# Optimization experiments

Hardware: AMD Instinct MI355X
Metric: run time of the kernel (lower is better)

## Reference

```python
import jax, jax.numpy as jnp
import numpy as np

B, S, HID = 2, 1024, 2048
H, D, KV = 32, 64, 8          # query heads, head dim, kv heads (GQA)
INNER = H * D                 # 2048
KV_DIM = KV * D               # 512


def setup_inputs() -> dict:
    key = jax.random.key(0)
    ks = jax.random.split(key, 12)
    s = 0.02
    return {
        "query": jax.random.normal(ks[0], (B, S, HID), jnp.float32),
        "key": jax.random.normal(ks[1], (B, S, HID), jnp.float32),
        "value": jax.random.normal(ks[2], (B, S, HID), jnp.float32),
        "mask": jnp.zeros((B, 1, S, S), jnp.float32),
        "position_bias": jax.random.normal(ks[3], (1, H, S, S), jnp.float32),
        "Wq": jax.random.normal(ks[4], (HID, INNER), jnp.float32) * s,
        "bq": jnp.zeros((INNER,), jnp.float32),
        "Wk": jax.random.normal(ks[5], (HID, KV_DIM), jnp.float32) * s,
        "bk": jnp.zeros((KV_DIM,), jnp.float32),
        "Wv": jax.random.normal(ks[6], (HID, KV_DIM), jnp.float32) * s,
        "bv": jnp.zeros((KV_DIM,), jnp.float32),
        "Wo": jax.random.normal(ks[7], (INNER, HID), jnp.float32) * s,
        "bo": jnp.zeros((HID,), jnp.float32),
    }


def reference(query, key, value, mask, position_bias, Wq, bq, Wk, bk, Wv, bv, Wo, bo):
    # projections (torch nn.Linear equivalent, weights stored [in,out])
    q = (query @ Wq + bq).reshape(B, S, H, D)     # [B,S,H,D]
    k = (key @ Wk + bk).reshape(B, S, KV, D)      # [B,S,KV,D]
    v = (value @ Wv + bv).reshape(B, S, KV, D)
    rep = H // KV
    k = jnp.repeat(k, rep, axis=2)                # GQA repeat_kv -> [B,S,H,D]
    v = jnp.repeat(v, rep, axis=2)
    scores = jnp.einsum("bqhd,bkhd->bhqk", q, k)  # [B,H,S,S]
    scores = (scores + position_bias) * (1.0 / jnp.sqrt(jnp.float32(D)))
    scores = scores + mask
    probs = jax.nn.softmax(scores.astype(jnp.float32), axis=-1).astype(q.dtype)
    out = jnp.einsum("bhqk,bkhd->bqhd", probs, v).reshape(B, S, INNER)
    return out @ Wo + bo                          # [B,S,HID]
```

## Files before the change

kernel.cpp:

```cpp
#include <hip/hip_runtime.h>
#include <stdint.h>


#define DEVI __device__ __forceinline__

typedef __attribute__((ext_vector_type(8))) short bf16x8;
typedef __attribute__((ext_vector_type(4))) float f32x4;
typedef __attribute__((ext_vector_type(4))) float flt4;
typedef __attribute__((ext_vector_type(8))) unsigned short u16x8;
typedef __attribute__((ext_vector_type(4))) unsigned short u16x4;

DEVI unsigned short f2bf(float f){
  union{float f;uint32_t u;}v; v.f=f;
  uint32_t u=v.u;
  u += 0x7FFFu + ((u>>16)&1u);
  return (unsigned short)(u>>16);
}

DEVI uint32_t cvt_pk_bf16(float lo, float hi){
  uint32_t r;
  asm("v_cvt_pk_bf16_f32 %0, %1, %2" : "=v"(r) : "v"(lo), "v"(hi));
  return r;
}

DEVI float fexp2(float x){
#if __has_builtin(__builtin_amdgcn_exp2f)
  return __builtin_amdgcn_exp2f(x);
#else
  return exp2f(x);
#endif
}

DEVI void gload16(const void* g, void* l){
  __builtin_amdgcn_global_load_lds((const __attribute__((address_space(1))) void*)g,
                                   (__attribute__((address_space(3))) void*)l, 16, 0, 0);
}

__global__ void prep_k(const float* __restrict__ q, const float* __restrict__ k,
                       const float* __restrict__ v,
                       unsigned short* __restrict__ qb, unsigned short* __restrict__ kb,
                       unsigned short* __restrict__ vb,
                       const float* __restrict__ Wq, const float* __restrict__ Wk,
                       const float* __restrict__ Wv, const float* __restrict__ Wo,
                       unsigned short* __restrict__ WqT, unsigned short* __restrict__ WkT,
                       unsigned short* __restrict__ WvT, unsigned short* __restrict__ WoT){
  __shared__ float tile[64][65];
  int bid = blockIdx.x;
  if (bid < 6144){
    int z = bid>>11;
    int i = (bid&2047)*256 + threadIdx.x;
    const float* src = z==0 ? q : (z==1 ? k : v);
    unsigned short* dst = z==0 ? qb : (z==1 ? kb : vb);
    const flt4* s = (const flt4*)src;
    flt4 a = s[2*i], b = s[2*i+1];
    u16x8 o;
    o[0]=f2bf(a.x); o[1]=f2bf(a.y); o[2]=f2bf(a.z); o[3]=f2bf(a.w);
    o[4]=f2bf(b.x); o[5]=f2bf(b.y); o[6]=f2bf(b.z); o[7]=f2bf(b.w);
    ((u16x8*)dst)[i] = o;
    return;
  }
  int id = bid - 6144;
  const int K = 2048;
  const float* W; unsigned short* WT; int N, tt;
  if (id < 1024)      { W=Wq; WT=WqT; N=2048; tt=id; }
  else if (id < 1280) { W=Wk; WT=WkT; N=512;  tt=id-1024; }
  else if (id < 1536) { W=Wv; WT=WvT; N=512;  tt=id-1280; }
  else                { W=Wo; WT=WoT; N=2048; tt=id-1536; }
  int sh = (N==2048) ? 5 : 3;
  int n0 = (tt & ((1<<sh)-1))*64, k0 = (tt >> sh)*64;
  int t = threadIdx.x;
  int r = t>>4, c4 = (t&15)*4;
  #pragma unroll
  for (int i=0;i<4;i++){
    flt4 vv = *(const flt4*)&W[(size_t)(k0 + r + i*16)*N + n0 + c4];
    tile[r+i*16][c4+0]=vv.x; tile[r+i*16][c4+1]=vv.y; tile[r+i*16][c4+2]=vv.z; tile[r+i*16][c4+3]=vv.w;
  }
  __syncthreads();
  #pragma unroll
  for (int i=0;i<4;i++){
    int rn = r + i*16;
    u16x4 o;
    o[0]=f2bf(tile[c4+0][rn]); o[1]=f2bf(tile[c4+1][rn]);
    o[2]=f2bf(tile[c4+2][rn]); o[3]=f2bf(tile[c4+3][rn]);
    *(u16x4*)&WT[(size_t)(n0+rn)*K + k0 + c4] = o;
  }
}

#define GEMM12864_KSTEP(A_, BT_, K_)                                           \
    __syncthreads();                                                           \
    _Pragma("unroll")                                                          \
    for (int j=0;j<4;j++){                                                     \
      int cid = (j*4+w)*64 + l;                                                \
      int row = cid>>3, sl = cid&7;                                            \
      int gsl = sl ^ (row&7);                                                  \
      gload16(&A_[(size_t)(m0+row)*K_ + k0 + gsl*8], &As[(j*4+w)*512]);        \
    }                                                                          \
    _Pragma("unroll")                                                          \
    for (int j=0;j<2;j++){                                                     \
      int cid = (j*4+w)*64 + l;                                                \
      int row = cid>>3, sl = cid&7;                                            \
      int gsl = sl ^ (row&7);                                                  \
      gload16(&BT_[(size_t)(n0+row)*K_ + k0 + gsl*8], &Bs[(j*4+w)*512]);       \
    }                                                                          \
    __syncthreads();                                                           \
    _Pragma("unroll")                                                          \
    for (int kk=0;kk<2;kk++){                                                  \
      bf16x8 af[2], bfv[4];                                                    \
      _Pragma("unroll")                                                        \
      for (int mt=0;mt<2;mt++){                                                \
        int row = wr+mt*16+lq;                                                 \
        af[mt] = *(const bf16x8*)&As[row*64 + (((kk*4+lg)^(lq&7))*8)];         \
      }                                                                        \
      _Pragma("unroll")                                                        \
      for (int nt=0;nt<4;nt++){                                                \
        int row = nt*16+lq;                                                    \
        bfv[nt] = *(const bf16x8*)&Bs[row*64 + (((kk*4+lg)^(lq&7))*8)];        \
      }                                                                        \
      _Pragma("unroll")                                                        \
      for (int mt=0;mt<2;mt++)                                                 \
        _Pragma("unroll")                                                      \
        for (int nt=0;nt<4;nt++)                                               \
          acc[mt][nt] = __builtin_amdgcn_mfma_f32_16x16x32_bf16(af[mt], bfv[nt], acc[mt][nt], 0,0,0); \
    }

__global__ __launch_bounds__(256,3) void qkv128(const unsigned short* __restrict__ qbf,
    const unsigned short* __restrict__ kbf, const unsigned short* __restrict__ vbf,
    const unsigned short* __restrict__ WqT, const unsigned short* __restrict__ WkT,
    const unsigned short* __restrict__ WvT,
    const float* __restrict__ bq, const float* __restrict__ bk, const float* __restrict__ bv,
    unsigned short* __restrict__ Qp, unsigned short* __restrict__ Kp, unsigned short* __restrict__ VTb){
  __shared__ unsigned short As[128*64];
  __shared__ unsigned short Bs[64*64];
  const int K = 2048;
  int id = blockIdx.x;
  const unsigned short *A, *BT; const float* bias; int N, op, tt;
  if (id < 512)      { op=0; A=qbf; BT=WqT; bias=bq; N=2048; tt=id; }
  else if (id < 640) { op=1; A=kbf; BT=WkT; bias=bk; N=512;  tt=id-512; }
  else               { op=2; A=vbf; BT=WvT; bias=bv; N=512;  tt=id-640; }
  int sh = (N==2048) ? 5 : 3;
  int n0 = (tt & ((1<<sh)-1))*64, m0 = (tt >> sh)*128;
  int t = threadIdx.x, w = t>>6, l = t&63;
  int lq = l&15, lg = l>>4;
  int wr = w*32;
  f32x4 acc[2][4] = {};
  for (int k0=0;k0<K;k0+=64){
    GEMM12864_KSTEP(A, BT, K)
  }
  #pragma unroll
  for (int nt=0;nt<4;nt++){
    int col = n0 + nt*16 + lq;
    float bvl = bias[col];
    #pragma unroll
    for (int mt=0;mt<2;mt++){
      #pragma unroll
      for (int r=0;r<4;r++){
        int row = m0 + wr + mt*16 + lg*4 + r;
        float v = acc[mt][nt][r] + bvl;
        if (op==0)      Qp[(size_t)row*2048 + col] = f2bf(v);
        else if (op==1) Kp[(size_t)row*512 + col] = f2bf(v);
        else {
          int b = row>>10, s = row&1023;
          VTb[((size_t)(b*512 + col)<<10) + s] = f2bf(v);
        }
      }
    }
  }
}

__global__ __launch_bounds__(256,3) void oproj128(const unsigned short* __restrict__ A,
    const unsigned short* __restrict__ BT, const float* __restrict__ bias,
    float* __restrict__ Cout){
  __shared__ unsigned short As[128*64];
  __shared__ unsigned short Bs[64*64];
  const int K = 2048, N = 2048;
  int n0 = blockIdx.x*64, m0 = blockIdx.y*128;
  int t = threadIdx.x, w = t>>6, l = t&63;
  int lq = l&15, lg = l>>4;
  int wr = w*32;
  f32x4 acc[2][4] = {};
  for (int k0=0;k0<K;k0+=64){
    GEMM12864_KSTEP(A, BT, K)
  }
  #pragma unroll
  for (int nt=0;nt<4;nt++){
    int col = n0 + nt*16 + lq;
    float bvl = bias[col];
    #pragma unroll
    for (int mt=0;mt<2;mt++){
      #pragma unroll
      for (int r=0;r<4;r++){
        int row = m0 + wr + mt*16 + lg*4 + r;
        Cout[(size_t)row*N + col] = acc[mt][nt][r] + bvl;
      }
    }
  }
}

__global__ __launch_bounds__(512,4) void attn_k(const unsigned short* __restrict__ Q,
    const unsigned short* __restrict__ Kp, const unsigned short* __restrict__ VT,
    const float* __restrict__ pbias, const float* __restrict__ mask,
    unsigned short* __restrict__ Oout){
  __shared__ unsigned short Ks[2][4096];
  __shared__ unsigned short VTs[2][4096];
  __shared__ float Ms[2][2048];
  __shared__ unsigned short Pb[8][1024];
  int t=threadIdx.x, w=t>>6, l=t&63;
  int phys = blockIdx.x;
  int lin = (phys&7)*64 + (phys>>3);
  int qb = lin>>4, kv = (lin>>1)&7, b = lin&1;
  int h = kv*4 + (w&3);
  int qhalf = w>>2;
  int lq = l&15, lg = l>>4;
  int q0 = qb*32 + qhalf*16;
  int mr = qhalf*16 + lq;
  bf16x8 qf0, qf1;
  {
    const unsigned short* qp = &Q[((size_t)(b*1024 + q0 + lq))*2048 + h*64 + lg*8];
    qf0 = *(const bf16x8*)qp;
    qf1 = *(const bf16x8*)(qp + 32);
  }
  const float* pbase  = &pbias[((size_t)h*1024 + (q0+lq))*1024];
  const float* maskWG = &mask [((size_t)(b*1024 + qb*32))*1024];
  f32x4 oacc[4] = {};
  float psum = 0.f;
  const float L2E   = 1.4426950408889634f;
  const float SCL2E = 0.125f*1.4426950408889634f;
  const float NFM   = -16.0f*1.4426950408889634f;
  unsigned short* pw = &Pb[w][0];
  int swz = (lq&7)<<3;

  flt4 RA[4], RB[4], comb[4];

#define ATTN_STAGE(buf_, kt_)                                                           \
  {                                                                                     \
    int c = w*64 + l;                                                                   \
    int krow = c>>3, ksl = (c&7)^(krow&7);                                              \
    gload16(&Kp[((size_t)(b*1024 + (kt_)*64 + krow))*512 + kv*64 + ksl*8], &Ks[buf_][w*512]);          \
    gload16(&VT[((size_t)(b*512 + kv*64 + krow))*1024 + (size_t)((kt_)*64 + ksl*8)], &VTs[buf_][w*512]);\
    int mrow = c>>4, msl = (c&15)^(mrow&7);                                             \
    gload16(&maskWG[(size_t)mrow*1024 + (kt_)*64 + msl*4], &Ms[buf_][w*256]);           \
  }

#define ATTN_RAW(RP_, kt_)                                                              \
  _Pragma("unroll")                                                                     \
  for (int nt=0;nt<4;nt++)                                                              \
    RP_[nt] = *(const flt4*)&pbase[(kt_)*64 + nt*16 + lg*4];

#define ATTN_COMBINE(RP_, cur_)                                                         \
  _Pragma("unroll")                                                                     \
  for (int nt=0;nt<4;nt++){                                                             \
    flt4 m4 = *(const flt4*)&Ms[cur_][mr*64 + (((nt*4+lg)^(mr&7))<<2)];                 \
    _Pragma("unroll")                                                                   \
    for (int r=0;r<4;r++)                                                               \
      comb[nt][r] = fmaf(RP_[nt][r], SCL2E, fmaf(m4[r], L2E, NFM));                     \
  }

#define ATTN_COMPUTE(P_)                                                                \
  {                                                                                     \
    f32x4 sacc[4] = {};                                                                 \
    __builtin_amdgcn_s_setprio(1);                                                      \
    _Pragma("unroll")                                                                   \
    for (int nt=0;nt<4;nt++){                                                           \
      int row = nt*16 + lq;                                                             \
      bf16x8 kf0 = *(const bf16x8*)&Ks[P_][row*64 + (( lg    ^ (row&7))*8)];            \
      bf16x8 kf1 = *(const bf16x8*)&Ks[P_][row*64 + (((4+lg) ^ (row&7))*8)];            \
      sacc[nt] = __builtin_amdgcn_mfma_f32_16x16x32_bf16(kf0, qf0, sacc[nt], 0,0,0);    \
      sacc[nt] = __builtin_amdgcn_mfma_f32_16x16x32_bf16(kf1, qf1, sacc[nt], 0,0,0);    \
    }                                                                                   \
    __builtin_amdgcn_s_setprio(0);                                                      \
    _Pragma("unroll")                                                                   \
    for (int nt=0;nt<4;nt++){                                                           \
      float p0 = fexp2(fmaf(sacc[nt][0], SCL2E, comb[nt][0]));                          \
      float p1 = fexp2(fmaf(sacc[nt][1], SCL2E, comb[nt][1]));                          \
      float p2 = fexp2(fmaf(sacc[nt][2], SCL2E, comb[nt][2]));                          \
      float p3 = fexp2(fmaf(sacc[nt][3], SCL2E, comb[nt][3]));                          \
      psum += (p0+p1)+(p2+p3);                                                          \
      uint2 pk;                                                                         \
      pk.x = cvt_pk_bf16(p0,p1);                                                        \
      pk.y = cvt_pk_bf16(p2,p3);                                                        \
      *(uint2*)&pw[lq*64 + ((nt*16 + lg*4) ^ swz)] = pk;                                \
    }                                                                                   \
    _Pragma("unroll")                                                                   \
    for (int kk=0;kk<2;kk++){                                                           \
      bf16x8 pa = *(const bf16x8*)&pw[lq*64 + ((kk*32 + lg*8) ^ swz)];                  \
      __builtin_amdgcn_s_setprio(1);                                                    \
      _Pragma("unroll")                                                                 \
      for (int nt=0;nt<4;nt++){                                                         \
        int vrow = nt*16 + lq;                                                          \
        bf16x8 vf = *(const bf16x8*)&VTs[P_][vrow*64 + (((kk*4+lg) ^ (vrow&7))*8)];     \
        oacc[nt] = __builtin_amdgcn_mfma_f32_16x16x32_bf16(pa, vf, oacc[nt], 0,0,0);    \
      }                                                                                 \
      __builtin_amdgcn_s_setprio(0);                                                    \
    }                                                                                   \
  }

#define TILE(kt_, cur_, RP_, DOSTAGE, DORAW, VMFULL)                                    \
  {                                                                                     \
    if (DOSTAGE) ATTN_STAGE((cur_)^1, (kt_)+1)                                          \
    if (VMFULL) { asm volatile("s_waitcnt vmcnt(7)" ::: "memory"); }                    \
    else        { asm volatile("s_waitcnt vmcnt(0)" ::: "memory"); }                    \
    __builtin_amdgcn_s_barrier();                                                       \
    ATTN_COMBINE(RP_, cur_)                                                             \
    if (DORAW) ATTN_RAW(RP_, (kt_)+2)                                                   \
    ATTN_COMPUTE(cur_)                                                                  \
    __builtin_amdgcn_s_barrier();                                                       \
  }

  ATTN_STAGE(0, 0)
  ATTN_RAW(RA, 0)
  ATTN_RAW(RB, 1)

  for (int kb=0; kb<14; kb+=2){
    TILE(kb+0, 0, RA, 1, 1, 1)
    TILE(kb+1, 1, RB, 1, 1, 1)
  }
  TILE(14, 0, RA, 1, 0, 1)
  TILE(15, 1, RB, 0, 0, 0)

  float lsum = psum;
  lsum += __shfl_xor(lsum, 16);
  lsum += __shfl_xor(lsum, 32);
  #pragma unroll
  for (int r=0;r<4;r++){
    float lr = __shfl(lsum, lg*4 + r);
    float linv = 1.f/lr;
    int qrow = q0 + lg*4 + r;
    #pragma unroll
    for (int nt=0;nt<4;nt++){
      Oout[((size_t)(b*1024 + qrow))*2048 + h*64 + nt*16 + lq] = f2bf(oacc[nt][r]*linv);
    }
  }
#undef TILE
#undef ATTN_COMPUTE
#undef ATTN_COMBINE
#undef ATTN_RAW
#undef ATTN_STAGE
}

extern "C" void kernel_launch(void* const* d_in, const int* in_sizes, int n_in,
                              void* d_out, int out_size, void* d_ws, size_t ws_size,
                              hipStream_t stream){
  (void)in_sizes; (void)n_in; (void)out_size; (void)ws_size;
  const float* query = (const float*)d_in[0];
  const float* key   = (const float*)d_in[1];
  const float* value = (const float*)d_in[2];
  const float* mask  = (const float*)d_in[3];
  const float* pbias = (const float*)d_in[4];
  const float* Wq = (const float*)d_in[5];
  const float* bq = (const float*)d_in[6];
  const float* Wk = (const float*)d_in[7];
  const float* bk = (const float*)d_in[8];
  const float* Wv = (const float*)d_in[9];
  const float* bv = (const float*)d_in[10];
  const float* Wo = (const float*)d_in[11];
  const float* bo = (const float*)d_in[12];
  char* ws = (char*)d_ws;
  const size_t MB = (size_t)1<<20;
  unsigned short* qbf = (unsigned short*)(ws + 0*MB);
  unsigned short* kbf = (unsigned short*)(ws + 8*MB);
  unsigned short* vbf = (unsigned short*)(ws + 16*MB);
  unsigned short* WqT = (unsigned short*)(ws + 24*MB);
  unsigned short* WkT = (unsigned short*)(ws + 32*MB);
  unsigned short* WvT = (unsigned short*)(ws + 34*MB);
  unsigned short* WoT = (unsigned short*)(ws + 36*MB);
  unsigned short* Qp  = (unsigned short*)(ws + 44*MB);
  unsigned short* Kp  = (unsigned short*)(ws + 52*MB);
  unsigned short* VTb = (unsigned short*)(ws + 54*MB);
  unsigned short* Aout= (unsigned short*)(ws + 56*MB);

  prep_k<<<8704,256,0,stream>>>(query, key, value, qbf, kbf, vbf,
                                Wq, Wk, Wv, Wo, WqT, WkT, WvT, WoT);
  qkv128<<<768,256,0,stream>>>(qbf, kbf, vbf, WqT, WkT, WvT, bq, bk, bv, Qp, Kp, VTb);
  attn_k<<<512,512,0,stream>>>(Qp, Kp, VTb, pbias, mask, Aout);
  oproj128<<<dim3(32,16),256,0,stream>>>(Aout, WoT, bo, (float*)d_out);
}
```

Measured before the change: 149.1 us.

## Double-buffer GEMM k-loop and convert mask to bf16 before attention

```diff
diff --git a/kernel.cpp b/kernel.cpp
--- a/kernel.cpp
+++ b/kernel.cpp
@@ -15,6 +15,10 @@
   uint32_t u=v.u;
   u += 0x7FFFu + ((u>>16)&1u);
   return (unsigned short)(u>>16);
+}
+
+DEVI float bf2f(unsigned short s){
+  union{uint32_t u;float f;}v; v.u = ((uint32_t)s)<<16; return v.f;
 }
 
 DEVI uint32_t cvt_pk_bf16(float lo, float hi){
@@ -37,20 +41,26 @@
 }
 
 __global__ void prep_k(const float* __restrict__ q, const float* __restrict__ k,
-                       const float* __restrict__ v,
+                       const float* __restrict__ v, const float* __restrict__ mk,
                        unsigned short* __restrict__ qb, unsigned short* __restrict__ kb,
-                       unsigned short* __restrict__ vb,
+                       unsigned short* __restrict__ vb, unsigned short* __restrict__ mb,
                        const float* __restrict__ Wq, const float* __restrict__ Wk,
                        const float* __restrict__ Wv, const float* __restrict__ Wo,
                        unsigned short* __restrict__ WqT, unsigned short* __restrict__ WkT,
                        unsigned short* __restrict__ WvT, unsigned short* __restrict__ WoT){
   __shared__ float tile[64][65];
   int bid = blockIdx.x;
-  if (bid < 6144){
-    int z = bid>>11;
-    int i = (bid&2047)*256 + threadIdx.x;
-    const float* src = z==0 ? q : (z==1 ? k : v);
-    unsigned short* dst = z==0 ? qb : (z==1 ? kb : vb);
+  if (bid < 7168){
+    const float* src; unsigned short* dst; int i;
+    if (bid < 6144){
+      int z = bid>>11;
+      i = (bid&2047)*256 + threadIdx.x;
+      src = z==0 ? q : (z==1 ? k : v);
+      dst = z==0 ? qb : (z==1 ? kb : vb);
+    } else {
+      i = (bid-6144)*256 + threadIdx.x;
+      src = mk; dst = mb;
+    }
     const flt4* s = (const flt4*)src;
     flt4 a = s[2*i], b = s[2*i+1];
     u16x8 o;
@@ -59,7 +69,7 @@
     ((u16x8*)dst)[i] = o;
     return;
   }
-  int id = bid - 6144;
+  int id = bid - 7168;
   const int K = 2048;
   const float* W; unsigned short* WT; int N, tt;
   if (id < 1024)      { W=Wq; WT=WqT; N=2048; tt=id; }
@@ -86,35 +96,35 @@
   }
 }
 
-#define GEMM12864_KSTEP(A_, BT_, K_)                                           \
-    __syncthreads();                                                           \
+#define G128_STAGE(buf_, k0_)                                                  \
     _Pragma("unroll")                                                          \
     for (int j=0;j<4;j++){                                                     \
       int cid = (j*4+w)*64 + l;                                                \
       int row = cid>>3, sl = cid&7;                                            \
       int gsl = sl ^ (row&7);                                                  \
-      gload16(&A_[(size_t)(m0+row)*K_ + k0 + gsl*8], &As[(j*4+w)*512]);        \
+      gload16(&A[(size_t)(m0+row)*K + (k0_) + gsl*8], &As[buf_][(j*4+w)*512]); \
     }                                                                          \
     _Pragma("unroll")                                                          \
     for (int j=0;j<2;j++){                                                     \
       int cid = (j*4+w)*64 + l;                                                \
       int row = cid>>3, sl = cid&7;                                            \
       int gsl = sl ^ (row&7);                                                  \
-      gload16(&BT_[(size_t)(n0+row)*K_ + k0 + gsl*8], &Bs[(j*4+w)*512]);       \
-    }                                                                          \
-    __syncthreads();                                                           \
+      gload16(&BT[(size_t)(n0+row)*K + (k0_) + gsl*8], &Bs[buf_][(j*4+w)*512]);\
+    }
+
+#define G128_COMPUTE(buf_)                                                     \
     _Pragma("unroll")                                                          \
     for (int kk=0;kk<2;kk++){                                                  \
       bf16x8 af[2], bfv[4];                                                    \
       _Pragma("unroll")                                                        \
       for (int mt=0;mt<2;mt++){                                                \
         int row = wr+mt*16+lq;                                                 \
-        af[mt] = *(const bf16x8*)&As[row*64 + (((kk*4+lg)^(lq&7))*8)];         \
+        af[mt] = *(const bf16x8*)&As[buf_][row*64 + (((kk*4+lg)^(lq&7))*8)];   \
       }                                                                        \
       _Pragma("unroll")                                                        \
       for (int nt=0;nt<4;nt++){                                                \
         int row = nt*16+lq;                                                    \
-        bfv[nt] = *(const bf16x8*)&Bs[row*64 + (((kk*4+lg)^(lq&7))*8)];        \
+        bfv[nt] = *(const bf16x8*)&Bs[buf_][row*64 + (((kk*4+lg)^(lq&7))*8)];  \
       }                                                                        \
       _Pragma("unroll")                                                        \
       for (int mt=0;mt<2;mt++)                                                 \
@@ -123,14 +133,29 @@
           acc[mt][nt] = __builtin_amdgcn_mfma_f32_16x16x32_bf16(af[mt], bfv[nt], acc[mt][nt], 0,0,0); \
     }
 
+#define G128_LOOP                                                              \
+  G128_STAGE(0, 0)                                                             \
+  for (int t32=0; t32<32; ++t32){                                              \
+    int cur = t32&1;                                                           \
+    if (t32 < 31){                                                             \
+      G128_STAGE(cur^1, (t32+1)*64)                                            \
+      asm volatile("s_waitcnt vmcnt(6)" ::: "memory");                         \
+    } else {                                                                   \
+      asm volatile("s_waitcnt vmcnt(0)" ::: "memory");                         \
+    }                                                                          \
+    __builtin_amdgcn_s_barrier();                                              \
+    G128_COMPUTE(cur)                                                          \
+    __builtin_amdgcn_s_barrier();                                              \
+  }
+
 __global__ __launch_bounds__(256,3) void qkv128(const unsigned short* __restrict__ qbf,
     const unsigned short* __restrict__ kbf, const unsigned short* __restrict__ vbf,
     const unsigned short* __restrict__ WqT, const unsigned short* __restrict__ WkT,
     const unsigned short* __restrict__ WvT,
     const float* __restrict__ bq, const float* __restrict__ bk, const float* __restrict__ bv,
     unsigned short* __restrict__ Qp, unsigned short* __restrict__ Kp, unsigned short* __restrict__ VTb){
-  __shared__ unsigned short As[128*64];
-  __shared__ unsigned short Bs[64*64];
+  __shared__ unsigned short As[2][128*64];
+  __shared__ unsigned short Bs[2][64*64];
   const int K = 2048;
   int id = blockIdx.x;
   const unsigned short *A, *BT; const float* bias; int N, op, tt;
@@ -143,9 +168,7 @@
   int lq = l&15, lg = l>>4;
   int wr = w*32;
   f32x4 acc[2][4] = {};
-  for (int k0=0;k0<K;k0+=64){
-    GEMM12864_KSTEP(A, BT, K)
-  }
+  G128_LOOP
   #pragma unroll
   for (int nt=0;nt<4;nt++){
     int col = n0 + nt*16 + lq;
@@ -170,17 +193,15 @@
 __global__ __launch_bounds__(256,3) void oproj128(const unsigned short* __restrict__ A,
     const unsigned short* __restrict__ BT, const float* __restrict__ bias,
     float* __restrict__ Cout){
-  __shared__ unsigned short As[128*64];
-  __shared__ unsigned short Bs[64*64];
+  __shared__ unsigned short As[2][128*64];
+  __shared__ unsigned short Bs[2][64*64];
   const int K = 2048, N = 2048;
   int n0 = blockIdx.x*64, m0 = blockIdx.y*128;
   int t = threadIdx.x, w = t>>6, l = t&63;
   int lq = l&15, lg = l>>4;
   int wr = w*32;
   f32x4 acc[2][4] = {};
-  for (int k0=0;k0<K;k0+=64){
-    GEMM12864_KSTEP(A, BT, K)
-  }
+  G128_LOOP
   #pragma unroll
   for (int nt=0;nt<4;nt++){
     int col = n0 + nt*16 + lq;
@@ -198,11 +219,11 @@
 
 __global__ __launch_bounds__(512,4) void attn_k(const unsigned short* __restrict__ Q,
     const unsigned short* __restrict__ Kp, const unsigned short* __restrict__ VT,
-    const float* __restrict__ pbias, const float* __restrict__ mask,
+    const float* __restrict__ pbias, const unsigned short* __restrict__ maskBF,
     unsigned short* __restrict__ Oout){
   __shared__ unsigned short Ks[2][4096];
   __shared__ unsigned short VTs[2][4096];
-  __shared__ float Ms[2][2048];
+  __shared__ unsigned short Ms[2][2048];
   __shared__ unsigned short Pb[8][1024];
   int t=threadIdx.x, w=t>>6, l=t&63;
   int phys = blockIdx.x;
@@ -219,8 +240,8 @@
     qf0 = *(const bf16x8*)qp;
     qf1 = *(const bf16x8*)(qp + 32);
   }
-  const float* pbase  = &pbias[((size_t)h*1024 + (q0+lq))*1024];
-  const float* maskWG = &mask [((size_t)(b*1024 + qb*32))*1024];
+  const float* pbase = &pbias[((size_t)h*1024 + (q0+lq))*1024];
+  const unsigned short* maskWG = &maskBF[((size_t)(b*1024 + qb*32))*1024];
   f32x4 oacc[4] = {};
   float psum = 0.f;
   const float L2E   = 1.4426950408889634f;
@@ -237,8 +258,11 @@
     int krow = c>>3, ksl = (c&7)^(krow&7);                                              \
     gload16(&Kp[((size_t)(b*1024 + (kt_)*64 + krow))*512 + kv*64 + ksl*8], &Ks[buf_][w*512]);          \
     gload16(&VT[((size_t)(b*512 + kv*64 + krow))*1024 + (size_t)((kt_)*64 + ksl*8)], &VTs[buf_][w*512]);\
-    int mrow = c>>4, msl = (c&15)^(mrow&7);                                             \
-    gload16(&maskWG[(size_t)mrow*1024 + (kt_)*64 + msl*4], &Ms[buf_][w*256]);           \
+    if (l < 32){                                                                        \
+      int cm = w*32 + l;                                                                \
+      int mrow = cm>>3, msl = (cm&7)^(mrow&7);                                          \
+      gload16(&maskWG[(size_t)mrow*1024 + (kt_)*64 + msl*8], &Ms[buf_][w*256]);         \
+    }                                                                                   \
   }
 
 #define ATTN_RAW(RP_, kt_)                                                              \
@@ -249,10 +273,11 @@
 #define ATTN_COMBINE(RP_, cur_)                                                         \
   _Pragma("unroll")                                                                     \
   for (int nt=0;nt<4;nt++){                                                             \
-    flt4 m4 = *(const flt4*)&Ms[cur_][mr*64 + (((nt*4+lg)^(mr&7))<<2)];                 \
+    int j = nt*4 + lg;                                                                  \
+    u16x4 mw = *(const u16x4*)&Ms[cur_][mr*64 + ((((j>>1)^(mr&7))<<3) + ((j&1)<<2))];   \
     _Pragma("unroll")                                                                   \
     for (int r=0;r<4;r++)                                                               \
-      comb[nt][r] = fmaf(RP_[nt][r], SCL2E, fmaf(m4[r], L2E, NFM));                     \
+      comb[nt][r] = fmaf(RP_[nt][r], SCL2E, fmaf(bf2f(mw[r]), L2E, NFM));               \
   }
 
 #define ATTN_COMPUTE(P_)                                                                \
@@ -357,6 +382,7 @@
   char* ws = (char*)d_ws;
   const size_t MB = (size_t)1<<20;
   unsigned short* qbf = (unsigned short*)(ws + 0*MB);
+  unsigned short* Aout= (unsigned short*)(ws + 0*MB);
   unsigned short* kbf = (unsigned short*)(ws + 8*MB);
   unsigned short* vbf = (unsigned short*)(ws + 16*MB);
   unsigned short* WqT = (unsigned short*)(ws + 24*MB);
@@ -366,11 +392,11 @@
   unsigned short* Qp  = (unsigned short*)(ws + 44*MB);
   unsigned short* Kp  = (unsigned short*)(ws + 52*MB);
   unsigned short* VTb = (unsigned short*)(ws + 54*MB);
-  unsigned short* Aout= (unsigned short*)(ws + 56*MB);
-
-  prep_k<<<8704,256,0,stream>>>(query, key, value, qbf, kbf, vbf,
+  unsigned short* mkBF= (unsigned short*)(ws + 56*MB);
+
+  prep_k<<<9728,256,0,stream>>>(query, key, value, mask, qbf, kbf, vbf, mkBF,
                                 Wq, Wk, Wv, Wo, WqT, WkT, WvT, WoT);
   qkv128<<<768,256,0,stream>>>(qbf, kbf, vbf, WqT, WkT, WvT, bq, bk, bv, Qp, Kp, VTb);
-  attn_k<<<512,512,0,stream>>>(Qp, Kp, VTb, pbias, mask, Aout);
+  attn_k<<<512,512,0,stream>>>(Qp, Kp, VTb, pbias, mkBF, Aout);
   oproj128<<<dim3(32,16),256,0,stream>>>(Aout, WoT, bo, (float*)d_out);
 }
```

New measurement: 154.0 us. 3.3% more time.
